# Performance work log

Hardware: AMD Instinct MI355X
Metric: run time of the kernel (lower is better)

Reference implementation:

```python
import jax, jax.numpy as jnp
import numpy as np

F_NODE = 32   # node feature dim
E_ATTR = 8    # edge attribute dim
H_OUT = 64    # h_theta output dim


def setup_inputs() -> dict:
    key = jax.random.key(0)
    k1, k2, k3 = jax.random.split(key, 3)
    B, N = 1, 1024
    adjacency = jax.random.randint(k1, (B, N, N), 0, 2, dtype=jnp.int32)
    node_features = jax.random.normal(k2, (B, N, F_NODE), dtype=jnp.float32)
    edge_attributes = jax.random.normal(k3, (B, N, N, E_ATTR), dtype=jnp.float32)
    kW = jax.random.fold_in(key, 7)
    W = jax.random.normal(kW, (2 * F_NODE + E_ATTR, H_OUT), dtype=jnp.float32) * (1.0 / np.sqrt(2 * F_NODE + E_ATTR))
    b = jnp.zeros((H_OUT,), dtype=jnp.float32)
    return {"adjacency": adjacency, "node_features": node_features,
            "edge_attributes": edge_attributes, "W": W, "b": b}


def reference(adjacency, node_features, edge_attributes, W, b):
    # EdgeConvE: per edge (v, v') compute h_theta(concat([x_v, x_v' - x_v, e_vv']))
    # then aggregate over neighbors v' selected by the dense adjacency.
    # Split W along the concat axis so we never materialize the [B,N,N,2F+E] concat:
    # concat @ W = x_v @ W_self + (x_v' - x_v) @ W_diff + e @ W_edge
    F = node_features.shape[-1]
    W_self, W_diff, W_edge = W[:F], W[F:2 * F], W[2 * F:]
    self_term = node_features @ (W_self - W_diff)            # [B,N,H]
    nbr_term = node_features @ W_diff                        # [B,N,H]
    edge_term = jnp.einsum('bvwe,eh->bvwh', edge_attributes, W_edge)  # [B,N,N,H]
    msg = jax.nn.relu(self_term[:, :, None, :] + nbr_term[:, None, :, :] + edge_term + b)
    A = adjacency.astype(msg.dtype)                          # [B,N,N] 0/1 mask
    out = jnp.einsum('bvw,bvwh->bvh', A, msg)                # sum-aggregate over neighbors
    return out
```

## Files before the change

### kernel.cpp

```cpp
#include <hip/hip_runtime.h>
#include <hip/hip_bf16.h>

#define N 1024
#define F 32
#define H 64
#define EA 8

typedef __attribute__((ext_vector_type(8))) short bf16x8;
typedef __attribute__((ext_vector_type(16))) float f32x16;

union FragAB { bf16x8 v; unsigned u[4]; };

__device__ __forceinline__ unsigned pk(float a, float b) {
    union { __hip_bfloat162 h; unsigned u; } c;
    c.h = __float22bfloat162_rn(float2{a, b});
    return c.u;
}

__global__ __launch_bounds__(256) void precompute_terms(
    const float* __restrict__ X, const float* __restrict__ W, const float* __restrict__ b,
    float* __restrict__ sv, float* __restrict__ nb, float* __restrict__ out)
{
    const int lane = threadIdx.x & 63;
    const int wid  = threadIdx.x >> 6;
    const int v    = blockIdx.x * 4 + wid;

    float4 xr[8];
    const float4* xp = (const float4*)(X + (size_t)v * F);
#pragma unroll
    for (int i = 0; i < 8; ++i) xr[i] = xp[i];
    const float* xf = (const float*)xr;

    float s = b[lane];
    float n = 0.f;
#pragma unroll
    for (int f = 0; f < F; ++f) {
        float ws = W[f * H + lane];
        float wd = W[(F + f) * H + lane];
        s = fmaf(xf[f], ws - wd, s);
        n = fmaf(xf[f], wd, n);
    }
    const int idx = v * H + lane;
    sv[idx]  = s;
    nb[idx]  = n;
    out[idx] = 0.f;
}

__global__ __launch_bounds__(256, 4) void edge_mfma(
    const int* __restrict__ A, const float* __restrict__ Edge, const float* __restrict__ W,
    const float* __restrict__ sv, const float* __restrict__ nb, float* __restrict__ out)
{
    const int lane = threadIdx.x & 63;
    const int wid  = threadIdx.x >> 6;
    const int lg   = lane >> 5;
    const int ln   = lane & 31;
    const int wq   = blockIdx.x & 7;
    const int vch  = blockIdx.x >> 3;
    const int wbase = wq * 128 + wid * 32;
    const int vbase = vch * 8;

    __shared__ float part[4][2][8][64];

    FragAB bfr[2];
#pragma unroll
    for (int half = 0; half < 2; ++half) {
        const int n = half * 32 + ln;
#pragma unroll
        for (int q = 0; q < 4; ++q) {
            unsigned we = pk(W[(2 * F + 2 * q) * H + n], W[(2 * F + 2 * q + 1) * H + n]);
            bfr[half].u[q] = (lg == 0) ? we : 0u;
        }
    }

    f32x16 cnb[2];
#pragma unroll
    for (int half = 0; half < 2; ++half)
#pragma unroll
        for (int r = 0; r < 16; ++r) {
            const int row = (r & 3) + 8 * (r >> 2) + 4 * lg;
            cnb[half][r] = nb[(size_t)(wbase + row) * H + half * 32 + ln];
        }

    const float4* ep = (const float4*)(Edge + ((size_t)vbase * N + wbase + ln) * EA);
    const int* ap = A + (size_t)vbase * N + wbase + ln;

    float4 eA = ep[0];
    float4 eB = ep[1];
    int    am = ap[0];

#pragma unroll
    for (int vi = 0; vi < 8; ++vi) {
        const float4 ca = eA;
        const float4 cb = eB;
        const int   cam = am;
        if (vi < 7) {
            eA = ep[(vi + 1) * 2048];
            eB = ep[(vi + 1) * 2048 + 1];
            am = ap[(size_t)(vi + 1) * N];
        }
        const int v = vbase + vi;
        const unsigned sp0 = pk(sv[(size_t)v * H + ln],      1e30f);
        const unsigned sp1 = pk(sv[(size_t)v * H + 32 + ln], 1e30f);

        FragAB afr;
        const unsigned mpat = cam ? 0x00003f80u : 0xbf803f80u;
        afr.u[0] = (lg == 0) ? pk(ca.x, ca.y) : mpat;
        afr.u[1] = (lg == 0) ? pk(ca.z, ca.w) : 0u;
        afr.u[2] = (lg == 0) ? pk(cb.x, cb.y) : 0u;
        afr.u[3] = (lg == 0) ? pk(cb.z, cb.w) : 0u;

        FragAB b0 = bfr[0], b1 = bfr[1];
        if (lg) { b0.u[0] = sp0; b1.u[0] = sp1; }

        const f32x16 d0 = __builtin_amdgcn_mfma_f32_32x32x16_bf16(afr.v, b0.v, cnb[0], 0, 0, 0);
        const f32x16 d1 = __builtin_amdgcn_mfma_f32_32x32x16_bf16(afr.v, b1.v, cnb[1], 0, 0, 0);

        float p0 = 0.f, p1 = 0.f;
#pragma unroll
        for (int r = 0; r < 16; ++r) {
            p0 += fmaxf(d0[r], 0.f);
            p1 += fmaxf(d1[r], 0.f);
        }
        part[wid][lg][vi][ln]      = p0;
        part[wid][lg][vi][32 + ln] = p1;
    }

    __syncthreads();
#pragma unroll
    for (int i = threadIdx.x; i < 512; i += 256) {
        const int vi = i >> 6, h = i & 63;
        float s = 0.f;
#pragma unroll
        for (int w4 = 0; w4 < 4; ++w4)
#pragma unroll
            for (int g = 0; g < 2; ++g) s += part[w4][g][vi][h];
        unsafeAtomicAdd(&out[(size_t)(vbase + vi) * H + h], s);
    }
}

extern "C" void kernel_launch(void* const* d_in, const int* in_sizes, int n_in,
                              void* d_out, int out_size, void* d_ws, size_t ws_size,
                              hipStream_t stream) {
    const int*   A    = (const int*)d_in[0];
    const float* X    = (const float*)d_in[1];
    const float* Edge = (const float*)d_in[2];
    const float* W    = (const float*)d_in[3];
    const float* b    = (const float*)d_in[4];
    float* out = (float*)d_out;

    float* sv = (float*)d_ws;
    float* nb = sv + N * H;

    precompute_terms<<<dim3(256), dim3(256), 0, stream>>>(X, W, b, sv, nb, out);
    edge_mfma<<<dim3(1024), dim3(256), 0, stream>>>(A, Edge, W, sv, nb, out);
}
```

Measured before the change: 89.58 us.

## Stage edge tiles into LDS via direct global loads and atomically add per wave

Each wave now issues direct global-to-LDS loads (global_load_lds) for all eight 1KB edge-attribute rows up front, preloads the adjacency and self-term values into registers, and waits once before the MFMA loop. The intent is to put all the memory traffic in flight at once instead of using a one-step register prefetch. The shared-memory partial buffer, the block barrier and the cross-wave reduction are removed. Each wave instead issues atomic adds straight to the output, which raises the atomic count about eightfold and risks contention on the same output rows.

```diff
diff --git a/kernel.cpp b/kernel.cpp
--- a/kernel.cpp
+++ b/kernel.cpp
@@ -10,6 +10,13 @@
 typedef __attribute__((ext_vector_type(16))) float f32x16;
 
 union FragAB { bf16x8 v; unsigned u[4]; };
+
+typedef const __attribute__((address_space(1))) void global_cv;
+typedef __attribute__((address_space(3))) void lds_v;
+
+__device__ __forceinline__ void stage_1kb(const float* g, float* l, int lane) {
+    __builtin_amdgcn_global_load_lds((global_cv*)(g + lane * 4), (lds_v*)l, 16, 0, 0);
+}
 
 __device__ __forceinline__ unsigned pk(float a, float b) {
     union { __hip_bfloat162 h; unsigned u; } c;
@@ -59,7 +66,20 @@
     const int wbase = wq * 128 + wid * 32;
     const int vbase = vch * 8;
 
-    __shared__ float part[4][2][8][64];
+    __shared__ float ebuf[4][8][256];
+
+    const float* eg = Edge + ((size_t)vbase * N + wbase) * EA;
+#pragma unroll
+    for (int vi = 0; vi < 8; ++vi)
+        stage_1kb(eg + (size_t)vi * N * EA, &ebuf[wid][vi][0], lane);
+
+    int am[8]; float s0v[8], s1v[8];
+#pragma unroll
+    for (int vi = 0; vi < 8; ++vi) {
+        am[vi]  = A[(size_t)(vbase + vi) * N + wbase + ln];
+        s0v[vi] = sv[(size_t)(vbase + vi) * H + ln];
+        s1v[vi] = sv[(size_t)(vbase + vi) * H + 32 + ln];
+    }
 
     FragAB bfr[2];
 #pragma unroll
@@ -81,36 +101,24 @@
             cnb[half][r] = nb[(size_t)(wbase + row) * H + half * 32 + ln];
         }
 
-    const float4* ep = (const float4*)(Edge + ((size_t)vbase * N + wbase + ln) * EA);
-    const int* ap = A + (size_t)vbase * N + wbase + ln;
-
-    float4 eA = ep[0];
-    float4 eB = ep[1];
-    int    am = ap[0];
+    __builtin_amdgcn_s_waitcnt(0);
+    __builtin_amdgcn_sched_barrier(0);
 
 #pragma unroll
     for (int vi = 0; vi < 8; ++vi) {
-        const float4 ca = eA;
-        const float4 cb = eB;
-        const int   cam = am;
-        if (vi < 7) {
-            eA = ep[(vi + 1) * 2048];
-            eB = ep[(vi + 1) * 2048 + 1];
-            am = ap[(size_t)(vi + 1) * N];
-        }
-        const int v = vbase + vi;
-        const unsigned sp0 = pk(sv[(size_t)v * H + ln],      1e30f);
-        const unsigned sp1 = pk(sv[(size_t)v * H + 32 + ln], 1e30f);
+        const float* eL = &ebuf[wid][vi][0];
+        const float4 ca = *(const float4*)&eL[ln * 8];
+        const float4 cb = *(const float4*)&eL[ln * 8 + 4];
 
         FragAB afr;
-        const unsigned mpat = cam ? 0x00003f80u : 0xbf803f80u;
+        const unsigned mpat = am[vi] ? 0x00003f80u : 0xbf803f80u;
         afr.u[0] = (lg == 0) ? pk(ca.x, ca.y) : mpat;
         afr.u[1] = (lg == 0) ? pk(ca.z, ca.w) : 0u;
         afr.u[2] = (lg == 0) ? pk(cb.x, cb.y) : 0u;
         afr.u[3] = (lg == 0) ? pk(cb.z, cb.w) : 0u;
 
         FragAB b0 = bfr[0], b1 = bfr[1];
-        if (lg) { b0.u[0] = sp0; b1.u[0] = sp1; }
+        if (lg) { b0.u[0] = pk(s0v[vi], 1e30f); b1.u[0] = pk(s1v[vi], 1e30f); }
 
         const f32x16 d0 = __builtin_amdgcn_mfma_f32_32x32x16_bf16(afr.v, b0.v, cnb[0], 0, 0, 0);
         const f32x16 d1 = __builtin_amdgcn_mfma_f32_32x32x16_bf16(afr.v, b1.v, cnb[1], 0, 0, 0);
@@ -121,20 +129,8 @@
             p0 += fmaxf(d0[r], 0.f);
             p1 += fmaxf(d1[r], 0.f);
         }
-        part[wid][lg][vi][ln]      = p0;
-        part[wid][lg][vi][32 + ln] = p1;
-    }
-
-    __syncthreads();
-#pragma unroll
-    for (int i = threadIdx.x; i < 512; i += 256) {
-        const int vi = i >> 6, h = i & 63;
-        float s = 0.f;
-#pragma unroll
-        for (int w4 = 0; w4 < 4; ++w4)
-#pragma unroll
-            for (int g = 0; g < 2; ++g) s += part[w4][g][vi][h];
-        unsafeAtomicAdd(&out[(size_t)(vbase + vi) * H + h], s);
+        unsafeAtomicAdd(&out[(size_t)(vbase + vi) * H + ln], p0);
+        unsafeAtomicAdd(&out[(size_t)(vbase + vi) * H + 32 + ln], p1);
     }
 }
 
```

New measurement: 133.6 us. 49.1% more time.
